# Performance work log

Measured on AMD Instinct MI355X. Metric: run time of the kernel, lower is better.

## Reference

```python
import jax, jax.numpy as jnp
import numpy as np

B, T, S, E, H = 8, 1024, 1024, 1024, 16
HS = E // H
FF = 4 * E
EPS = 1e-5


def layernorm(x, g, b):
    mu = jnp.mean(x, axis=-1, keepdims=True)
    var = jnp.mean(jnp.square(x - mu), axis=-1, keepdims=True)
    return (x - mu) * jax.lax.rsqrt(var + EPS) * g + b


def mha(q_in, k_in, v_in, Wq, Wk, Wv, Wo, bo, mask4):
    # Wq/Wk/Wv: [E, E] with columns grouped per head (equivalent to the
    # per-head nn.Linear weights concatenated along the output dim).
    Bq, Tq, _ = q_in.shape
    Tk = k_in.shape[1]
    q = (q_in @ Wq).reshape(Bq, Tq, H, HS)
    k = (k_in @ Wk).reshape(Bq, Tk, H, HS)
    v = (v_in @ Wv).reshape(Bq, Tk, H, HS)
    scores = jnp.einsum('bqhd,bkhd->bhqk', q, k) * (HS ** -0.5)
    scores = jnp.where(mask4, scores, -jnp.inf)
    attn = jax.nn.softmax(scores, axis=-1)  # dropout is identity in eval
    out = jnp.einsum('bhqk,bkhd->bqhd', attn, v).reshape(Bq, Tq, E)
    return out @ Wo + bo


def setup_inputs() -> dict:
    key = jax.random.key(0)
    ks = jax.random.split(key, 12)
    sd = E ** -0.5
    inp = {
        'x': jax.random.normal(ks[0], (B, T, E), jnp.float32),
        'enc_out': jax.random.normal(ks[1], (B, S, E), jnp.float32),
        'tgt_mask': jnp.ones((B, T), dtype=bool),
        'src_mask': jnp.ones((B, S), dtype=bool),
        'ln1_g': jnp.ones((E,), jnp.float32), 'ln1_b': jnp.zeros((E,), jnp.float32),
        'ln2_g': jnp.ones((E,), jnp.float32), 'ln2_b': jnp.zeros((E,), jnp.float32),
        'ln3_g': jnp.ones((E,), jnp.float32), 'ln3_b': jnp.zeros((E,), jnp.float32),
        'Wq_s': jax.random.normal(ks[2], (E, E), jnp.float32) * sd,
        'Wk_s': jax.random.normal(ks[3], (E, E), jnp.float32) * sd,
        'Wv_s': jax.random.normal(ks[4], (E, E), jnp.float32) * sd,
        'Wo_s': jax.random.normal(ks[5], (E, E), jnp.float32) * sd,
        'bo_s': jnp.zeros((E,), jnp.float32),
        'Wq_c': jax.random.normal(ks[6], (E, E), jnp.float32) * sd,
        'Wk_c': jax.random.normal(ks[7], (E, E), jnp.float32) * sd,
        'Wv_c': jax.random.normal(ks[8], (E, E), jnp.float32) * sd,
        'Wo_c': jax.random.normal(ks[9], (E, E), jnp.float32) * sd,
        'bo_c': jnp.zeros((E,), jnp.float32),
        'W1': jax.random.normal(ks[10], (E, FF), jnp.float32) * sd,
        'b1': jnp.zeros((FF,), jnp.float32),
        'W2': jax.random.normal(ks[11], (FF, E), jnp.float32) * (FF ** -0.5),
        'b2': jnp.zeros((E,), jnp.float32),
    }
    return inp


def reference(x, enc_out, tgt_mask, src_mask,
              ln1_g, ln1_b, ln2_g, ln2_b, ln3_g, ln3_b,
              Wq_s, Wk_s, Wv_s, Wo_s, bo_s,
              Wq_c, Wk_c, Wv_c, Wo_c, bo_c,
              W1, b1, W2, b2):
    Tq = x.shape[1]
    # vectorized equivalent of the Python double-loop: causal AND key-padding
    causal = jnp.tril(jnp.ones((Tq, Tq), dtype=bool))  # [T,T]
    self_mask = (tgt_mask[:, None, :] & causal[None])[:, None, :, :]  # [B,1,T,T]
    cross_mask = src_mask[:, None, None, :]  # [B,1,1,S] broadcasts to [B,H,T,S]

    h1 = layernorm(x, ln1_g, ln1_b)
    x = x + mha(h1, h1, h1, Wq_s, Wk_s, Wv_s, Wo_s, bo_s, self_mask)
    h2 = layernorm(x, ln2_g, ln2_b)
    x = x + mha(h2, enc_out, enc_out, Wq_c, Wk_c, Wv_c, Wo_c, bo_c, cross_mask)
    h3 = layernorm(x, ln3_g, ln3_b)
    ff = jax.nn.relu(h3 @ W1 + b1) @ W2 + b2  # dropout identity in eval
    return x + ff
```

## Files before the change

kernel.cpp:

```cpp
#include <hip/hip_runtime.h>

typedef unsigned short u16;
typedef __attribute__((ext_vector_type(8))) short bf16x8;
typedef __attribute__((ext_vector_type(4))) float f32x4;

__device__ __forceinline__ float bf2f(u16 u) {
    return __uint_as_float(((unsigned)u) << 16);
}
__device__ __forceinline__ u16 f2bf(float f) {
    unsigned u = __float_as_uint(f);
    u = (u + 0x7fffu + ((u >> 16) & 1u)) >> 16;
    return (u16)u;
}
__device__ __forceinline__ u16 f2bf_fast(float f) {
    return (u16)((__float_as_uint(f) + 0x8000u) >> 16);
}
__device__ __forceinline__ float fexp2(float x) { return __builtin_amdgcn_exp2f(x); }
__device__ __forceinline__ void gld_lds16(const u16* g, u16* l) {
    __builtin_amdgcn_global_load_lds(
        (const __attribute__((address_space(1))) void*)g,
        (__attribute__((address_space(3))) void*)l, 16, 0, 0);
}
__device__ __forceinline__ unsigned lds_off(const u16* p) {
    return (unsigned)(unsigned long long)(const __attribute__((address_space(3))) u16*)p;
}
__device__ __forceinline__ void barrier_() {
    asm volatile("" ::: "memory");
    __builtin_amdgcn_s_barrier();
    asm volatile("" ::: "memory");
}
#define VMCNT(n) asm volatile("s_waitcnt vmcnt(" #n ")" ::: "memory")
#define LGKM(n) do { \
    asm volatile("s_waitcnt lgkmcnt(" #n ")" ::: "memory"); \
    __builtin_amdgcn_sched_barrier(0); \
} while(0)
#define DSR(dst, addr) asm volatile("ds_read_b128 %0, %1" : "=v"(dst) : "v"(addr))

__global__ __launch_bounds__(256) void convert_f32_bf16(
    const float* __restrict__ in, u16* __restrict__ out) {
    long i = ((long)blockIdx.x * 256 + threadIdx.x) * 4;
    float4 v = *(const float4*)&in[i];
    alignas(8) u16 o[4] = {f2bf(v.x), f2bf(v.y), f2bf(v.z), f2bf(v.w)};
    *(uint2*)&out[i] = *(const uint2*)o;
}

__device__ __forceinline__ void transpose_w_body(
    const float* __restrict__ in, u16* __restrict__ out, int R, int C) {
    __shared__ u16 tile[64][72];
    int r0 = blockIdx.y * 64, c0 = blockIdx.x * 64;
    int tid = threadIdx.x;
#pragma unroll
    for (int it = 0; it < 4; ++it) {
        int f = it * 1024 + tid * 4;
        int r = f >> 6, c = f & 63;
        float4 v = *(const float4*)&in[(long)(r0 + r) * C + (c0 + c)];
        alignas(8) u16 o[4] = {f2bf(v.x), f2bf(v.y), f2bf(v.z), f2bf(v.w)};
        *(uint2*)&tile[r][c] = *(const uint2*)o;
    }
    __syncthreads();
#pragma unroll
    for (int it = 0; it < 2; ++it) {
        int f = it * 2048 + tid * 8;
        int rr = f >> 6, cc = f & 63;
        alignas(16) u16 tmp[8];
#pragma unroll
        for (int i = 0; i < 8; ++i) tmp[i] = tile[cc + i][rr];
        *(uint4*)&out[(long)(c0 + rr) * R + (r0 + cc)] = *(const uint4*)tmp;
    }
}

__global__ __launch_bounds__(256) void transpose_w(
    const float* __restrict__ in, u16* __restrict__ out, int R, int C) {
    transpose_w_body(in, out, R, C);
}

__global__ __launch_bounds__(256) void transpose_w4(
    const float* __restrict__ p0, const float* __restrict__ p1,
    const float* __restrict__ p2, const float* __restrict__ p3,
    u16* __restrict__ out) {
    int z = blockIdx.z;
    const float* in = (z == 0) ? p0 : (z == 1) ? p1 : (z == 2) ? p2 : p3;
    transpose_w_body(in, out + (long)z * 1024 * 1024, 1024, 1024);
}

__global__ __launch_bounds__(256) void transpose_b(
    const u16* __restrict__ in, u16* __restrict__ out,
    int R, int C, int istride, long ibs, long obs) {
    __shared__ u16 tile[64][72];
    const u16* src = in + (long)blockIdx.z * ibs;
    u16* dst = out + (long)blockIdx.z * obs;
    int r0 = blockIdx.y * 64, c0 = blockIdx.x * 64;
    int tid = threadIdx.x;
#pragma unroll
    for (int it = 0; it < 2; ++it) {
        int f = it * 2048 + tid * 8;
        int r = f >> 6, c = f & 63;
        *(uint4*)&tile[r][c] = *(const uint4*)&src[(long)(r0 + r) * istride + (c0 + c)];
    }
    __syncthreads();
#pragma unroll
    for (int it = 0; it < 2; ++it) {
        int f = it * 2048 + tid * 8;
        int rr = f >> 6, cc = f & 63;
        alignas(16) u16 tmp[8];
#pragma unroll
        for (int i = 0; i < 8; ++i) tmp[i] = tile[cc + i][rr];
        *(uint4*)&dst[(long)(c0 + rr) * R + (r0 + cc)] = *(const uint4*)tmp;
    }
}

__global__ __launch_bounds__(256) void ln_kernel(
    const float* __restrict__ x, const float* __restrict__ g,
    const float* __restrict__ bta, u16* __restrict__ y) {
    long row = blockIdx.x;
    int tid = threadIdx.x;
    float4 v4 = *(const float4*)&x[row * 1024 + tid * 4];
    float v[4] = {v4.x, v4.y, v4.z, v4.w};
    float s = 0.f, ss = 0.f;
#pragma unroll
    for (int i = 0; i < 4; ++i) { s += v[i]; ss += v[i] * v[i]; }
#pragma unroll
    for (int o = 1; o < 64; o <<= 1) { s += __shfl_xor(s, o, 64); ss += __shfl_xor(ss, o, 64); }
    __shared__ float red[8];
    int wv = tid >> 6, lane = tid & 63;
    if (lane == 0) { red[wv] = s; red[4 + wv] = ss; }
    __syncthreads();
    s = red[0] + red[1] + red[2] + red[3];
    ss = red[4] + red[5] + red[6] + red[7];
    float mean = s * (1.f / 1024.f);
    float var = ss * (1.f / 1024.f) - mean * mean;
    float rs = rsqrtf(var + 1e-5f);
    float4 g4 = *(const float4*)&g[tid * 4];
    float4 b4 = *(const float4*)&bta[tid * 4];
    float gg[4] = {g4.x, g4.y, g4.z, g4.w};
    float bb[4] = {b4.x, b4.y, b4.z, b4.w};
    alignas(8) u16 o4[4];
#pragma unroll
    for (int i = 0; i < 4; ++i)
        o4[i] = f2bf((v[i] - mean) * rs * gg[i] + bb[i]);
    *(uint2*)&y[row * 1024 + tid * 4] = *(const uint2*)o4;
}

#define STA(b,t,h) do { \
    gld_lds16(Ag + ((h)*128 +  0) * (long)K + (t)*64, AsL + (b)*16384 + (h)*8192); \
    gld_lds16(Ag + ((h)*128 + 64) * (long)K + (t)*64, AsL + (b)*16384 + (h)*8192 + 4096); \
} while(0)
#define STB(b,t,h) do { \
    gld_lds16(Bg + ((h)*128 +  0) * (long)K + (t)*64, BsL + (b)*16384 + (h)*8192); \
    gld_lds16(Bg + ((h)*128 + 64) * (long)K + (t)*64, BsL + (b)*16384 + (h)*8192 + 4096); \
} while(0)
#define RDB(b) do { \
    DSR(bfr[0][0], aB0 + (b)*32768 +    0); DSR(bfr[0][1], aB1 + (b)*32768 +    0); \
    DSR(bfr[1][0], aB0 + (b)*32768 + 2048); DSR(bfr[1][1], aB1 + (b)*32768 + 2048); \
    DSR(bfr[2][0], aB0 + (b)*32768 + 4096); DSR(bfr[2][1], aB1 + (b)*32768 + 4096); \
    DSR(bfr[3][0], aB0 + (b)*32768 + 6144); DSR(bfr[3][1], aB1 + (b)*32768 + 6144); \
} while(0)
#define RDA(b,q) do { \
    DSR(a0, aA0 + (b)*32768 + (2*(q)  )*2048); \
    DSR(a1, aA1 + (b)*32768 + (2*(q)  )*2048); \
    DSR(a2, aA0 + (b)*32768 + (2*(q)+1)*2048); \
    DSR(a3, aA1 + (b)*32768 + (2*(q)+1)*2048); \
} while(0)
#define MM(q) do { \
    __builtin_amdgcn_s_setprio(1); \
    _Pragma("unroll") \
    for (int j = 0; j < 4; ++j) { \
        acc[2*(q)  ][j] = __builtin_amdgcn_mfma_f32_16x16x32_bf16(a0, bfr[j][0], acc[2*(q)  ][j], 0, 0, 0); \
        acc[2*(q)  ][j] = __builtin_amdgcn_mfma_f32_16x16x32_bf16(a1, bfr[j][1], acc[2*(q)  ][j], 0, 0, 0); \
        acc[2*(q)+1][j] = __builtin_amdgcn_mfma_f32_16x16x32_bf16(a2, bfr[j][0], acc[2*(q)+1][j], 0, 0, 0); \
        acc[2*(q)+1][j] = __builtin_amdgcn_mfma_f32_16x16x32_bf16(a3, bfr[j][1], acc[2*(q)+1][j], 0, 0, 0); } \
    __builtin_amdgcn_s_setprio(0); \
} while(0)

__device__ __forceinline__ void supertile_map(int id, long& bm, long& bn) {
    int c = id & 7, j = id >> 3;
    int k = j >> 4, off = j & 15;
    bm = (long)(c * 4 + (off & 3)) * 256;
    bn = (long)(k * 4 + (off >> 2)) * 256;
}

template<int BIAS, int RES, int RELU, int OUTF32, int SPLITK>
__device__ __forceinline__ void gemm256_body(
    const u16* __restrict__ A, const u16* __restrict__ Bt,
    const float* __restrict__ bias, const float* __restrict__ res,
    void* __restrict__ Cv, long bm, long bn, int K, int kLen, int koff,
    int ldc, int kz, u16* As, u16* Bs) {
    int tid = threadIdx.x;
    int lane = tid & 63;
    int l15 = lane & 15, quad = lane >> 4;
    int wv = tid >> 6, wm = wv >> 2, wn = wv & 3;
    int NT = kLen >> 6, NI = NT >> 1;

    int srow = tid >> 3;
    int scol = ((tid & 7) ^ (srow & 7)) << 3;
    const u16* Ag = A + (bm + srow) * (long)K + koff + scol;
    const u16* Bg = Bt + (bn + srow) * (long)K + koff + scol;
    u16* AsL = As + tid * 8;
    u16* BsL = Bs + tid * 8;

    int c0 = (quad * 8) ^ ((l15 & 7) << 3);
    int c1 = (32 + quad * 8) ^ ((l15 & 7) << 3);
    unsigned arB = lds_off(As + (wm * 128 + l15) * 64);
    unsigned brB = lds_off(Bs + (wn * 64 + l15) * 64);
    unsigned aA0 = arB + 2 * c0, aA1 = arB + 2 * c1;
    unsigned aB0 = brB + 2 * c0, aB1 = brB + 2 * c1;

    f32x4 zf = {0.f, 0.f, 0.f, 0.f};
    f32x4 acc[8][4];
#pragma unroll
    for (int i = 0; i < 8; ++i)
#pragma unroll
        for (int j = 0; j < 4; ++j) acc[i][j] = zf;

    STA(0,0,0); STA(0,0,1); STB(0,0,0); STB(0,0,1); STB(1,1,0); STB(1,1,1);
    VMCNT(4);
    barrier_();

    bf16x8 bfr[4][2];
    bf16x8 a0, a1, a2, a3;

#pragma unroll 1
    for (int it2 = 0; it2 < NI; ++it2) {
        int t = 2 * it2, t1 = t + 1;
        int ts2 = (t + 2 < NT) ? t + 2 : t;
        int ts3 = (t + 3 < NT) ? t + 3 : t1;
        RDB(0); RDA(0,0); STA(1,t1,0); STA(1,t1,1);
            barrier_(); LGKM(0); MM(0); barrier_();
        RDA(0,1); STB(0,ts2,0);
            barrier_(); LGKM(0); MM(1); barrier_();
        RDA(0,2); STB(0,ts2,1);
            barrier_(); LGKM(0); MM(2); barrier_();
        RDA(0,3); VMCNT(4);
            barrier_(); LGKM(0); MM(3); barrier_();
        RDB(1); RDA(1,0); STA(0,ts2,0); STA(0,ts2,1);
            barrier_(); LGKM(0); MM(0); barrier_();
        RDA(1,1); STB(1,ts3,0);
            barrier_(); LGKM(0); MM(1); barrier_();
        RDA(1,2); STB(1,ts3,1);
            barrier_(); LGKM(0); MM(2); barrier_();
        RDA(1,3); VMCNT(4);
            barrier_(); LGKM(0); MM(3); barrier_();
    }
    VMCNT(0);

    long row0 = bm + wm * 128 + quad * 4;
    long col0 = bn + wn * 64 + l15;
#pragma unroll
    for (int i = 0; i < 8; ++i) {
        long row = row0 + i * 16;
#pragma unroll
        for (int j = 0; j < 4; ++j) {
            long col = col0 + j * 16;
            float bv = (BIAS && (!SPLITK || kz == 0)) ? bias[col] : 0.f;
#pragma unroll
            for (int r = 0; r < 4; ++r) {
                float v = acc[i][j][r] + bv;
                if (RES) v += res[(row + r) * ldc + col];
                if (RELU) v = fmaxf(v, 0.f);
                if (SPLITK) atomicAdd(&((float*)Cv)[(row + r) * ldc + col], v);
                else if (OUTF32) ((float*)Cv)[(row + r) * ldc + col] = v;
                else ((u16*)Cv)[(row + r) * ldc + col] = f2bf(v);
            }
        }
    }
}

template<int BIAS, int RES, int RELU, int OUTF32, int SPLITK>
__global__ __launch_bounds__(512) void gemm256(
    const u16* __restrict__ A, const u16* __restrict__ Bt,
    const float* __restrict__ bias, const float* __restrict__ res,
    void* __restrict__ Cv, int tilesM, int K, int ldc) {
    __shared__ u16 As[2 * 256 * 64];
    __shared__ u16 Bs[2 * 256 * 64];
    (void)tilesM;
    long bm, bn;
    supertile_map(blockIdx.x, bm, bn);
    int kLen = SPLITK ? (K >> 1) : K;
    int koff = SPLITK ? ((int)blockIdx.y * kLen) : 0;
    gemm256_body<BIAS, RES, RELU, OUTF32, SPLITK>(
        A, Bt, bias, res, Cv, bm, bn, K, kLen, koff, ldc, blockIdx.y, As, Bs);
}

__global__ __launch_bounds__(512) void gemm256_cross(
    const u16* __restrict__ hq, const u16* __restrict__ encb,
    const u16* __restrict__ wT, u16* __restrict__ qbuf, u16* __restrict__ kv) {
    __shared__ u16 As[2 * 256 * 64];
    __shared__ u16 Bs[2 * 256 * 64];
    int id = blockIdx.x;
    const u16* A; const u16* Bt; u16* C; int ldc;
    if (id < 128) { A = hq; Bt = wT; C = qbuf; ldc = 1024; }
    else { id -= 128; A = encb; Bt = wT + 1024l * 1024l; C = kv; ldc = 2048; }
    long bm, bn;
    supertile_map(id, bm, bn);
    gemm256_body<0, 0, 0, 0, 0>(
        A, Bt, nullptr, nullptr, C, bm, bn, 1024, 1024, 0, ldc, 0, As, Bs);
}

template<bool CAUSAL>
__global__ __launch_bounds__(256) void attn_kernel(
    const u16* __restrict__ q, const u16* __restrict__ k,
    const u16* __restrict__ vT, u16* __restrict__ out, int qld, int kld) {
    __shared__ u16 Qs[64][72];
    __shared__ u16 Ks[64][72];
    __shared__ u16 VTs[64][72];
    __shared__ u16 Ps[4][16][72];
    const int S_ = 1024;
    int qt = CAUSAL ? (gridDim.x - 1 - blockIdx.x) : blockIdx.x;
    int h = blockIdx.y, b = blockIdx.z;
    int tid = threadIdx.x, lane = tid & 63, wv = tid >> 6;
    int l15 = lane & 15, quad = lane >> 4;
    long qbase = ((long)b * 1024 + qt * 64) * qld + h * 64;
    long obase = ((long)b * 1024 + qt * 64) * 1024 + h * 64;
#pragma unroll
    for (int it = 0; it < 2; ++it) {
        int f = it * 2048 + tid * 8;
        int r = f >> 6, c = f & 63;
        *(uint4*)&Qs[r][c] = *(const uint4*)&q[qbase + (long)r * qld + c];
    }
    __syncthreads();
    bf16x8 a0 = *(const bf16x8*)&Qs[wv * 16 + l15][quad * 8];
    bf16x8 a1 = *(const bf16x8*)&Qs[wv * 16 + l15][quad * 8 + 32];
    f32x4 zf = {0.f, 0.f, 0.f, 0.f};
    f32x4 O[4];
#pragma unroll
    for (int j = 0; j < 4; ++j) O[j] = zf;
    const float cs = 0.125f * 1.44269504089f;
    float m_run = -3e30f;
    float lp[4] = {0.f, 0.f, 0.f, 0.f};
    long kbase = (long)b * 1024 * kld + h * 64;
    long vtbase = ((long)b * 16 + h) * 64 * (long)S_;
    int ktmax = CAUSAL ? qt : (S_ / 64 - 1);

    for (int kt = 0; kt <= ktmax; ++kt) {
        __syncthreads();
#pragma unroll
        for (int it = 0; it < 2; ++it) {
            int f = it * 2048 + tid * 8;
            int r = f >> 6, c = f & 63;
            *(uint4*)&Ks[r][c]  = *(const uint4*)&k[kbase + (long)(kt * 64 + r) * kld + c];
            *(uint4*)&VTs[r][c] = *(const uint4*)&vT[vtbase + (long)r * S_ + kt * 64 + c];
        }
        __syncthreads();

        f32x4 s[4];
#pragma unroll
        for (int j = 0; j < 4; ++j) {
            bf16x8 kb0 = *(const bf16x8*)&Ks[j * 16 + l15][quad * 8];
            bf16x8 kb1 = *(const bf16x8*)&Ks[j * 16 + l15][quad * 8 + 32];
            f32x4 z = zf;
            z = __builtin_amdgcn_mfma_f32_16x16x32_bf16(a0, kb0, z, 0, 0, 0);
            z = __builtin_amdgcn_mfma_f32_16x16x32_bf16(a1, kb1, z, 0, 0, 0);
            s[j] = z;
        }
        if (CAUSAL && kt == qt) {
#pragma unroll
            for (int j = 0; j < 4; ++j)
#pragma unroll
                for (int r = 0; r < 4; ++r)
                    if ((j * 16 + l15) > (wv * 16 + quad * 4 + r)) s[j][r] = -3e30f;
        }
        float mx = s[0][0];
#pragma unroll
        for (int j = 0; j < 4; ++j)
#pragma unroll
            for (int r = 0; r < 4; ++r) mx = fmaxf(mx, s[j][r]);
#pragma unroll
        for (int o = 1; o < 64; o <<= 1) mx = fmaxf(mx, __shfl_xor(mx, o, 64));
        float mn = fmaxf(m_run, mx);
        bool grew = mn > m_run;
        if (grew) {
            float alpha = fexp2((m_run - mn) * cs);
            m_run = mn;
#pragma unroll
            for (int j = 0; j < 4; ++j) {
                O[j][0] *= alpha; O[j][1] *= alpha; O[j][2] *= alpha; O[j][3] *= alpha;
            }
#pragma unroll
            for (int r = 0; r < 4; ++r) lp[r] *= alpha;
        }
        float mc = m_run * cs;
#pragma unroll
        for (int j = 0; j < 4; ++j)
#pragma unroll
            for (int r = 0; r < 4; ++r) {
                float p = fexp2(__builtin_fmaf(s[j][r], cs, -mc));
                lp[r] += p;
                Ps[wv][quad * 4 + r][j * 16 + l15] = f2bf_fast(p);
            }
        bf16x8 pa0 = *(const bf16x8*)&Ps[wv][l15][quad * 8];
        bf16x8 pa1 = *(const bf16x8*)&Ps[wv][l15][quad * 8 + 32];
#pragma unroll
        for (int j = 0; j < 4; ++j) {
            bf16x8 vb0 = *(const bf16x8*)&VTs[j * 16 + l15][quad * 8];
            bf16x8 vb1 = *(const bf16x8*)&VTs[j * 16 + l15][quad * 8 + 32];
            f32x4 o = O[j];
            o = __builtin_amdgcn_mfma_f32_16x16x32_bf16(pa0, vb0, o, 0, 0, 0);
            o = __builtin_amdgcn_mfma_f32_16x16x32_bf16(pa1, vb1, o, 0, 0, 0);
            O[j] = o;
        }
    }
#pragma unroll
    for (int r = 0; r < 4; ++r) {
#pragma unroll
        for (int o = 1; o < 16; o <<= 1) lp[r] += __shfl_xor(lp[r], o, 64);
        lp[r] = 1.f / lp[r];
    }
#pragma unroll
    for (int j = 0; j < 4; ++j)
#pragma unroll
        for (int r = 0; r < 4; ++r)
            out[obase + (long)(wv * 16 + quad * 4 + r) * 1024 + j * 16 + l15] =
                f2bf(O[j][r] * lp[r]);
}

extern "C" void kernel_launch(void* const* d_in, const int* in_sizes, int n_in,
                              void* d_out, int out_size, void* d_ws, size_t ws_size,
                              hipStream_t stream) {
    (void)in_sizes; (void)n_in; (void)out_size; (void)ws_size;
    const float* x    = (const float*)d_in[0];
    const float* enc  = (const float*)d_in[1];
    const float* ln1g = (const float*)d_in[4];
    const float* ln1b = (const float*)d_in[5];
    const float* ln2g = (const float*)d_in[6];
    const float* ln2b = (const float*)d_in[7];
    const float* ln3g = (const float*)d_in[8];
    const float* ln3b = (const float*)d_in[9];
    const float* Wq_s = (const float*)d_in[10];
    const float* Wk_s = (const float*)d_in[11];
    const float* Wv_s = (const float*)d_in[12];
    const float* Wo_s = (const float*)d_in[13];
    const float* bo_s = (const float*)d_in[14];
    const float* Wq_c = (const float*)d_in[15];
    const float* Wk_c = (const float*)d_in[16];
    const float* Wv_c = (const float*)d_in[17];
    const float* Wo_c = (const float*)d_in[18];
    const float* bo_c = (const float*)d_in[19];
    const float* W1   = (const float*)d_in[20];
    const float* b1   = (const float*)d_in[21];
    const float* W2   = (const float*)d_in[22];
    const float* b2   = (const float*)d_in[23];
    float* out = (float*)d_out;

    const long MEG = 1024l * 1024l;
    u16* ws0  = (u16*)d_ws;
    u16* hbuf = ws0 + 0 * MEG;
    u16* qkv  = ws0 + 8 * MEG;
    u16* qbuf = ws0 + 8 * MEG;
    u16* kv   = ws0 + 16 * MEG;
    u16* vTb  = ws0 + 32 * MEG;
    u16* encb = ws0 + 32 * MEG;
    u16* wT   = ws0 + 40 * MEG;
    u16* wT3  = ws0 + 43 * MEG;
    float* x1 = (float*)(ws0 + 44 * MEG);
    u16* ff1  = qkv;
    u16* w1T  = ws0 + 44 * MEG;
    u16* w2T  = ws0 + 48 * MEG;

    dim3 blk(256);
    dim3 blk5(512);
    dim3 gW4(16, 16, 4);
    dim3 gA(16, 16, 8);

    transpose_w4<<<gW4, blk, 0, stream>>>(Wq_s, Wk_s, Wv_s, Wo_s, wT);
    ln_kernel<<<8192, blk, 0, stream>>>(x, ln1g, ln1b, hbuf);
    gemm256<0,0,0,0,0><<<384, blk5, 0, stream>>>(hbuf, wT, nullptr, nullptr, qkv, 32, 1024, 3072);
    transpose_b<<<gA, blk, 0, stream>>>(qkv + 2048, vTb, 1024, 1024, 3072, 1024l * 3072, MEG);
    attn_kernel<true><<<gA, blk, 0, stream>>>(qkv, qkv + 1024, vTb, hbuf, 3072, 3072);
    gemm256<1,1,0,1,0><<<128, blk5, 0, stream>>>(hbuf, wT3, bo_s, x, x1, 32, 1024, 1024);

    transpose_w4<<<gW4, blk, 0, stream>>>(Wq_c, Wk_c, Wv_c, Wo_c, wT);
    ln_kernel<<<8192, blk, 0, stream>>>(x1, ln2g, ln2b, hbuf);
    convert_f32_bf16<<<8192, blk, 0, stream>>>(enc, encb);
    gemm256_cross<<<384, blk5, 0, stream>>>(hbuf, encb, wT, qbuf, kv);
    transpose_b<<<gA, blk, 0, stream>>>(kv + 1024, vTb, 1024, 1024, 2048, 1024l * 2048, MEG);
    attn_kernel<false><<<gA, blk, 0, stream>>>(qbuf, kv, vTb, hbuf, 1024, 2048);
    gemm256<1,1,0,1,0><<<128, blk5, 0, stream>>>(hbuf, wT3, bo_c, x1, out, 32, 1024, 1024);

    transpose_w<<<dim3(64, 16, 1), blk, 0, stream>>>(W1, w1T, 1024, 4096);
    transpose_w<<<dim3(16, 64, 1), blk, 0, stream>>>(W2, w2T, 4096, 1024);
    ln_kernel<<<8192, blk, 0, stream>>>(out, ln3g, ln3b, hbuf);
    gemm256<1,0,1,0,0><<<512, blk5, 0, stream>>>(hbuf, w1T, b1, nullptr, ff1, 32, 1024, 4096);
    gemm256<1,0,0,1,1><<<dim3(128, 2), blk5, 0, stream>>>(ff1, w2T, b2, nullptr, out, 32, 4096, 1024);
}
```

Before: 751.2 us.

## Template GEMM on N-tile width, drop split-K, fuse V-transpose into QKV epilogue

Makes the 256-row GEMM generic over the N-tile width (NJ) and uses 256x128 tiles for the output projections and FF2 GEMMs, which doubles their block count (256 instead of 128) without split-K atomics. FF2 now adds the residual directly instead of accumulating atomically into out. The self-attention QKV GEMM writes the V slice straight into the transposed vT layout, removing a separate transpose kernel. The narrower tiles mean less reuse per block, and the transposed V stores are strided.

Result: faster. 713.0 us (-5.1%).

```diff
diff --git a/kernel.cpp b/kernel.cpp
--- a/kernel.cpp
+++ b/kernel.cpp
@@ -141,82 +141,82 @@
     *(uint2*)&y[row * 1024 + tid * 4] = *(const uint2*)o4;
 }
 
-#define STA(b,t,h) do { \
-    gld_lds16(Ag + ((h)*128 +  0) * (long)K + (t)*64, AsL + (b)*16384 + (h)*8192); \
-    gld_lds16(Ag + ((h)*128 + 64) * (long)K + (t)*64, AsL + (b)*16384 + (h)*8192 + 4096); \
-} while(0)
-#define STB(b,t,h) do { \
-    gld_lds16(Bg + ((h)*128 +  0) * (long)K + (t)*64, BsL + (b)*16384 + (h)*8192); \
-    gld_lds16(Bg + ((h)*128 + 64) * (long)K + (t)*64, BsL + (b)*16384 + (h)*8192 + 4096); \
-} while(0)
-#define RDB(b) do { \
-    DSR(bfr[0][0], aB0 + (b)*32768 +    0); DSR(bfr[0][1], aB1 + (b)*32768 +    0); \
-    DSR(bfr[1][0], aB0 + (b)*32768 + 2048); DSR(bfr[1][1], aB1 + (b)*32768 + 2048); \
-    DSR(bfr[2][0], aB0 + (b)*32768 + 4096); DSR(bfr[2][1], aB1 + (b)*32768 + 4096); \
-    DSR(bfr[3][0], aB0 + (b)*32768 + 6144); DSR(bfr[3][1], aB1 + (b)*32768 + 6144); \
-} while(0)
-#define RDA(b,q) do { \
+#define STAF(b,t) do { _Pragma("unroll") \
+    for (int l = 0; l < 4; ++l) \
+        gld_lds16(Ag + (l * 64) * (long)K + (t) * 64, AsL + (b) * 16384 + l * 4096); \
+} while(0)
+#define STBF(b,t) do { _Pragma("unroll") \
+    for (int l = 0; l < NJ; ++l) \
+        gld_lds16(Bg + (l * 64) * (long)K + (t) * 64, BsL + (b) * (NJ * 4096) + l * 4096); \
+} while(0)
+#define RDBX(b) do { _Pragma("unroll") \
+    for (int j = 0; j < NJ; ++j) { \
+        DSR(bfr[j][0], aB0 + (b) * (NJ * 8192) + j * 2048); \
+        DSR(bfr[j][1], aB1 + (b) * (NJ * 8192) + j * 2048); } \
+} while(0)
+#define RDAX(b,q) do { \
     DSR(a0, aA0 + (b)*32768 + (2*(q)  )*2048); \
     DSR(a1, aA1 + (b)*32768 + (2*(q)  )*2048); \
     DSR(a2, aA0 + (b)*32768 + (2*(q)+1)*2048); \
     DSR(a3, aA1 + (b)*32768 + (2*(q)+1)*2048); \
 } while(0)
-#define MM(q) do { \
+#define MMX(q) do { \
     __builtin_amdgcn_s_setprio(1); \
     _Pragma("unroll") \
-    for (int j = 0; j < 4; ++j) { \
+    for (int j = 0; j < NJ; ++j) { \
         acc[2*(q)  ][j] = __builtin_amdgcn_mfma_f32_16x16x32_bf16(a0, bfr[j][0], acc[2*(q)  ][j], 0, 0, 0); \
         acc[2*(q)  ][j] = __builtin_amdgcn_mfma_f32_16x16x32_bf16(a1, bfr[j][1], acc[2*(q)  ][j], 0, 0, 0); \
         acc[2*(q)+1][j] = __builtin_amdgcn_mfma_f32_16x16x32_bf16(a2, bfr[j][0], acc[2*(q)+1][j], 0, 0, 0); \
         acc[2*(q)+1][j] = __builtin_amdgcn_mfma_f32_16x16x32_bf16(a3, bfr[j][1], acc[2*(q)+1][j], 0, 0, 0); } \
     __builtin_amdgcn_s_setprio(0); \
 } while(0)
-
-__device__ __forceinline__ void supertile_map(int id, long& bm, long& bn) {
+#define VMCNTNJ() do { if constexpr (NJ == 4) { VMCNT(4); } else { VMCNT(2); } } while(0)
+
+__device__ __forceinline__ void supertile_map(int id, int bnw, long& bm, long& bn) {
     int c = id & 7, j = id >> 3;
     int k = j >> 4, off = j & 15;
     bm = (long)(c * 4 + (off & 3)) * 256;
-    bn = (long)(k * 4 + (off >> 2)) * 256;
-}
-
-template<int BIAS, int RES, int RELU, int OUTF32, int SPLITK>
-__device__ __forceinline__ void gemm256_body(
+    bn = (long)(k * 4 + (off >> 2)) * bnw;
+}
+
+template<int NJ, int BIAS, int RES, int RELU, int OUTF32>
+__device__ __forceinline__ void gemm_body(
     const u16* __restrict__ A, const u16* __restrict__ Bt,
     const float* __restrict__ bias, const float* __restrict__ res,
-    void* __restrict__ Cv, long bm, long bn, int K, int kLen, int koff,
-    int ldc, int kz, u16* As, u16* Bs) {
+    void* __restrict__ Cv, long bm, long bn, int K, int ldc,
+    int vtcol, u16* __restrict__ vout, u16* As, u16* Bs) {
     int tid = threadIdx.x;
     int lane = tid & 63;
     int l15 = lane & 15, quad = lane >> 4;
     int wv = tid >> 6, wm = wv >> 2, wn = wv & 3;
-    int NT = kLen >> 6, NI = NT >> 1;
+    int NT = K >> 6, NI = NT >> 1;
 
     int srow = tid >> 3;
     int scol = ((tid & 7) ^ (srow & 7)) << 3;
-    const u16* Ag = A + (bm + srow) * (long)K + koff + scol;
-    const u16* Bg = Bt + (bn + srow) * (long)K + koff + scol;
+    const u16* Ag = A + (bm + srow) * (long)K + scol;
+    const u16* Bg = Bt + (bn + srow) * (long)K + scol;
     u16* AsL = As + tid * 8;
     u16* BsL = Bs + tid * 8;
 
     int c0 = (quad * 8) ^ ((l15 & 7) << 3);
     int c1 = (32 + quad * 8) ^ ((l15 & 7) << 3);
     unsigned arB = lds_off(As + (wm * 128 + l15) * 64);
-    unsigned brB = lds_off(Bs + (wn * 64 + l15) * 64);
+    unsigned brB = lds_off(Bs + (wn * (NJ * 16) + l15) * 64);
     unsigned aA0 = arB + 2 * c0, aA1 = arB + 2 * c1;
     unsigned aB0 = brB + 2 * c0, aB1 = brB + 2 * c1;
 
     f32x4 zf = {0.f, 0.f, 0.f, 0.f};
-    f32x4 acc[8][4];
+    f32x4 acc[8][NJ];
 #pragma unroll
     for (int i = 0; i < 8; ++i)
 #pragma unroll
-        for (int j = 0; j < 4; ++j) acc[i][j] = zf;
-
-    STA(0,0,0); STA(0,0,1); STB(0,0,0); STB(0,0,1); STB(1,1,0); STB(1,1,1);
-    VMCNT(4);
+        for (int j = 0; j < NJ; ++j) acc[i][j] = zf;
+
+    STAF(0,0); STBF(0,0); STBF(1,1);
+    VMCNTNJ();
     barrier_();
 
-    bf16x8 bfr[4][2];
+    bf16x8 bfr[NJ][2];
     bf16x8 a0, a1, a2, a3;
 
 #pragma unroll 1
@@ -224,76 +224,83 @@
         int t = 2 * it2, t1 = t + 1;
         int ts2 = (t + 2 < NT) ? t + 2 : t;
         int ts3 = (t + 3 < NT) ? t + 3 : t1;
-        RDB(0); RDA(0,0); STA(1,t1,0); STA(1,t1,1);
-            barrier_(); LGKM(0); MM(0); barrier_();
-        RDA(0,1); STB(0,ts2,0);
-            barrier_(); LGKM(0); MM(1); barrier_();
-        RDA(0,2); STB(0,ts2,1);
-            barrier_(); LGKM(0); MM(2); barrier_();
-        RDA(0,3); VMCNT(4);
-            barrier_(); LGKM(0); MM(3); barrier_();
-        RDB(1); RDA(1,0); STA(0,ts2,0); STA(0,ts2,1);
-            barrier_(); LGKM(0); MM(0); barrier_();
-        RDA(1,1); STB(1,ts3,0);
-            barrier_(); LGKM(0); MM(1); barrier_();
-        RDA(1,2); STB(1,ts3,1);
-            barrier_(); LGKM(0); MM(2); barrier_();
-        RDA(1,3); VMCNT(4);
-            barrier_(); LGKM(0); MM(3); barrier_();
+        RDBX(0); RDAX(0,0); STAF(1,t1);
+            barrier_(); LGKM(0); MMX(0); barrier_();
+        RDAX(0,1); STBF(0,ts2);
+            barrier_(); LGKM(0); MMX(1); barrier_();
+        RDAX(0,2);
+            barrier_(); LGKM(0); MMX(2); barrier_();
+        RDAX(0,3); VMCNTNJ();
+            barrier_(); LGKM(0); MMX(3); barrier_();
+        RDBX(1); RDAX(1,0); STAF(0,ts2);
+            barrier_(); LGKM(0); MMX(0); barrier_();
+        RDAX(1,1); STBF(1,ts3);
+            barrier_(); LGKM(0); MMX(1); barrier_();
+        RDAX(1,2);
+            barrier_(); LGKM(0); MMX(2); barrier_();
+        RDAX(1,3); VMCNTNJ();
+            barrier_(); LGKM(0); MMX(3); barrier_();
     }
     VMCNT(0);
 
     long row0 = bm + wm * 128 + quad * 4;
-    long col0 = bn + wn * 64 + l15;
+    long col0 = bn + wn * (NJ * 16) + l15;
 #pragma unroll
     for (int i = 0; i < 8; ++i) {
         long row = row0 + i * 16;
 #pragma unroll
-        for (int j = 0; j < 4; ++j) {
+        for (int j = 0; j < NJ; ++j) {
             long col = col0 + j * 16;
-            float bv = (BIAS && (!SPLITK || kz == 0)) ? bias[col] : 0.f;
-#pragma unroll
-            for (int r = 0; r < 4; ++r) {
-                float v = acc[i][j][r] + bv;
-                if (RES) v += res[(row + r) * ldc + col];
-                if (RELU) v = fmaxf(v, 0.f);
-                if (SPLITK) atomicAdd(&((float*)Cv)[(row + r) * ldc + col], v);
-                else if (OUTF32) ((float*)Cv)[(row + r) * ldc + col] = v;
-                else ((u16*)Cv)[(row + r) * ldc + col] = f2bf(v);
+            if (vtcol >= 0 && col >= vtcol) {
+                long vcol = col - vtcol;
+                int hh = (int)(vcol >> 6), d = (int)(vcol & 63);
+                int bb = (int)(row >> 10), s = (int)(row & 1023);
+                alignas(8) u16 o4[4];
+#pragma unroll
+                for (int r = 0; r < 4; ++r) o4[r] = f2bf(acc[i][j][r]);
+                *(uint2*)(vout + (((long)(bb * 16 + hh) * 64 + d) << 10) + s) =
+                    *(const uint2*)o4;
+            } else {
+                float bv = BIAS ? bias[col] : 0.f;
+#pragma unroll
+                for (int r = 0; r < 4; ++r) {
+                    float v = acc[i][j][r] + bv;
+                    if (RES) v += res[(row + r) * ldc + col];
+                    if (RELU) v = fmaxf(v, 0.f);
+                    if (OUTF32) ((float*)Cv)[(row + r) * ldc + col] = v;
+                    else ((u16*)Cv)[(row + r) * ldc + col] = f2bf(v);
+                }
             }
         }
     }
 }
 
-template<int BIAS, int RES, int RELU, int OUTF32, int SPLITK>
-__global__ __launch_bounds__(512) void gemm256(
+template<int NJ, int BIAS, int RES, int RELU, int OUTF32>
+__global__ __launch_bounds__(512) void gemm_k(
     const u16* __restrict__ A, const u16* __restrict__ Bt,
     const float* __restrict__ bias, const float* __restrict__ res,
-    void* __restrict__ Cv, int tilesM, int K, int ldc) {
-    __shared__ u16 As[2 * 256 * 64];
-    __shared__ u16 Bs[2 * 256 * 64];
-    (void)tilesM;
+    void* __restrict__ Cv, int K, int ldc, int vtcol, u16* __restrict__ vout) {
+    __shared__ u16 As[2 * 16384];
+    __shared__ u16 Bs[2 * NJ * 4096];
     long bm, bn;
-    supertile_map(blockIdx.x, bm, bn);
-    int kLen = SPLITK ? (K >> 1) : K;
-    int koff = SPLITK ? ((int)blockIdx.y * kLen) : 0;
-    gemm256_body<BIAS, RES, RELU, OUTF32, SPLITK>(
-        A, Bt, bias, res, Cv, bm, bn, K, kLen, koff, ldc, blockIdx.y, As, Bs);
-}
-
-__global__ __launch_bounds__(512) void gemm256_cross(
+    supertile_map(blockIdx.x, NJ * 64, bm, bn);
+    gemm_body<NJ, BIAS, RES, RELU, OUTF32>(
+        A, Bt, bias, res, Cv, bm, bn, K, ldc, vtcol, vout, As, Bs);
+}
+
+__global__ __launch_bounds__(512) void gemm_cross(
     const u16* __restrict__ hq, const u16* __restrict__ encb,
     const u16* __restrict__ wT, u16* __restrict__ qbuf, u16* __restrict__ kv) {
-    __shared__ u16 As[2 * 256 * 64];
-    __shared__ u16 Bs[2 * 256 * 64];
+    __shared__ u16 As[2 * 16384];
+    __shared__ u16 Bs[2 * 16384];
     int id = blockIdx.x;
     const u16* A; const u16* Bt; u16* C; int ldc;
     if (id < 128) { A = hq; Bt = wT; C = qbuf; ldc = 1024; }
     else { id -= 128; A = encb; Bt = wT + 1024l * 1024l; C = kv; ldc = 2048; }
     long bm, bn;
-    supertile_map(id, bm, bn);
-    gemm256_body<0, 0, 0, 0, 0>(
-        A, Bt, nullptr, nullptr, C, bm, bn, 1024, 1024, 0, ldc, 0, As, Bs);
+    supertile_map(id, 256, bm, bn);
+    gemm_body<4, 0, 0, 0, 0>(
+        A, Bt, nullptr, nullptr, C, bm, bn, 1024, ldc, -1, nullptr, As, Bs);
 }
 
 template<bool CAUSAL>
@@ -463,22 +470,21 @@
 
     transpose_w4<<<gW4, blk, 0, stream>>>(Wq_s, Wk_s, Wv_s, Wo_s, wT);
     ln_kernel<<<8192, blk, 0, stream>>>(x, ln1g, ln1b, hbuf);
-    gemm256<0,0,0,0,0><<<384, blk5, 0, stream>>>(hbuf, wT, nullptr, nullptr, qkv, 32, 1024, 3072);
-    transpose_b<<<gA, blk, 0, stream>>>(qkv + 2048, vTb, 1024, 1024, 3072, 1024l * 3072, MEG);
+    gemm_k<4,0,0,0,0><<<384, blk5, 0, stream>>>(hbuf, wT, nullptr, nullptr, qkv, 1024, 3072, 2048, vTb);
     attn_kernel<true><<<gA, blk, 0, stream>>>(qkv, qkv + 1024, vTb, hbuf, 3072, 3072);
-    gemm256<1,1,0,1,0><<<128, blk5, 0, stream>>>(hbuf, wT3, bo_s, x, x1, 32, 1024, 1024);
+    gemm_k<2,1,1,0,1><<<256, blk5, 0, stream>>>(hbuf, wT3, bo_s, x, x1, 1024, 1024, -1, nullptr);
 
     transpose_w4<<<gW4, blk, 0, stream>>>(Wq_c, Wk_c, Wv_c, Wo_c, wT);
     ln_kernel<<<8192, blk, 0, stream>>>(x1, ln2g, ln2b, hbuf);
     convert_f32_bf16<<<8192, blk, 0, stream>>>(enc, encb);
-    gemm256_cross<<<384, blk5, 0, stream>>>(hbuf, encb, wT, qbuf, kv);
+    gemm_cross<<<384, blk5, 0, stream>>>(hbuf, encb, wT, qbuf, kv);
     transpose_b<<<gA, blk, 0, stream>>>(kv + 1024, vTb, 1024, 1024, 2048, 1024l * 2048, MEG);
     attn_kernel<false><<<gA, blk, 0, stream>>>(qbuf, kv, vTb, hbuf, 1024, 2048);
-    gemm256<1,1,0,1,0><<<128, blk5, 0, stream>>>(hbuf, wT3, bo_c, x1, out, 32, 1024, 1024);
+    gemm_k<2,1,1,0,1><<<256, blk5, 0, stream>>>(hbuf, wT3, bo_c, x1, out, 1024, 1024, -1, nullptr);
 
     transpose_w<<<dim3(64, 16, 1), blk, 0, stream>>>(W1, w1T, 1024, 4096);
     transpose_w<<<dim3(16, 64, 1), blk, 0, stream>>>(W2, w2T, 4096, 1024);
     ln_kernel<<<8192, blk, 0, stream>>>(out, ln3g, ln3b, hbuf);
-    gemm256<1,0,1,0,0><<<512, blk5, 0, stream>>>(hbuf, w1T, b1, nullptr, ff1, 32, 1024, 4096);
-    gemm256<1,0,0,1,1><<<dim3(128, 2), blk5, 0, stream>>>(ff1, w2T, b2, nullptr, out, 32, 4096, 1024);
-}
+    gemm_k<4,1,0,1,0><<<512, blk5, 0, stream>>>(hbuf, w1T, b1, nullptr, ff1, 1024, 4096, -1, nullptr);
+    gemm_k<2,1,1,0,1><<<256, blk5, 0, stream>>>(ff1, w2T, b2, out, out, 4096, 1024, -1, nullptr);
+}
```
